# Kernel optimization log

Measured on AMD Instinct MI355X. Metric: run time of the kernel, lower is better.

Reference implementation:

```python
import jax, jax.numpy as jnp
import numpy as np

B, LQ, LK, D = 4, 2048, 2048, 512
EPS = 1e-8  # torch cosine_similarity eps


def setup_inputs() -> dict:
    key = jax.random.key(0)
    ks = jax.random.split(key, 8)
    s = 1.0 / np.sqrt(D)
    return {
        "query": jax.random.normal(ks[0], (B, LQ, D), jnp.float32),
        "key": jax.random.normal(ks[1], (B, LK, D), jnp.float32),
        "value": jax.random.normal(ks[2], (B, LK, D), jnp.float32),
        "Wq": jax.random.normal(ks[3], (D, D), jnp.float32) * s,
        "bq": jax.random.normal(ks[4], (D,), jnp.float32) * s,
        "Wk": jax.random.normal(ks[5], (D, D), jnp.float32) * s,
        "bk": jax.random.normal(ks[6], (D,), jnp.float32) * s,
        "scoring_weights": jnp.ones((3,), jnp.float32) / 3.0,
    }


def reference(query, key, value, Wq, bq, Wk, bk, scoring_weights):
    # fused tanh-QK transforms (torch Linear: x @ W.T + b)
    q = jnp.tanh(jnp.einsum('bqd,ed->bqe', query, Wq) + bq)  # [B,LQ,D]
    k = jnp.tanh(jnp.einsum('bkd,ed->bke', key, Wk) + bk)    # [B,LK,D]

    dot = jnp.einsum('bqd,bkd->bqk', q, k)                   # [B,LQ,LK]
    qn = jnp.linalg.norm(q, axis=-1)                         # [B,LQ]
    kn = jnp.linalg.norm(k, axis=-1)                         # [B,LK]
    # cosine_similarity: dot / max(|q|*|k|, eps)
    cos = dot / jnp.maximum(qn[:, :, None] * kn[:, None, :], EPS)
    # -cdist (p=2): sqrt(|q|^2 + |k|^2 - 2 q.k), clamped at 0
    sq = jnp.maximum(qn[:, :, None] ** 2 + kn[:, None, :] ** 2 - 2.0 * dot, 0.0)
    euc = -jnp.sqrt(sq)

    w = jax.nn.softmax(scoring_weights)
    scores = w[0] * dot + w[1] * cos + w[2] * euc
    attn = jax.nn.softmax(scores, axis=-1)                   # [B,LQ,LK]
    context = jnp.einsum('bqk,bkd->bqd', attn, value)        # [B,LQ,D]
    return context, attn
```

## Files before the change

### kernel.cpp

```cpp
#include <hip/hip_runtime.h>
#include <cstdint>
#include <cstddef>

namespace {

constexpr int BATCH = 4;
constexpr int LQ = 2048;
constexpr int LK = 2048;
constexpr int D = 512;
constexpr int MQ = BATCH * LQ;

using f16 = _Float16;
typedef _Float16 f16x8 __attribute__((ext_vector_type(8)));
typedef _Float16 f16x4 __attribute__((ext_vector_type(4)));
typedef float f32x4 __attribute__((ext_vector_type(4)));

__device__ __forceinline__ f16x8 cvt8(const float4 a, const float4 b) {
  f16x8 h;
  h[0] = (f16)a.x; h[1] = (f16)a.y; h[2] = (f16)a.z; h[3] = (f16)a.w;
  h[4] = (f16)b.x; h[5] = (f16)b.y; h[6] = (f16)b.z; h[7] = (f16)b.w;
  return h;
}

typedef __attribute__((address_space(1))) const void gas_void;
typedef __attribute__((address_space(3))) void las_void;
__device__ __forceinline__ void gload_lds16(const void* g, void* l) {
  __builtin_amdgcn_global_load_lds((gas_void*)g, (las_void*)l, 16, 0, 0);
}

__global__ __launch_bounds__(256) void prep_kernel(
    const float* __restrict__ query, const float* __restrict__ keyp,
    const float* __restrict__ value, const float* __restrict__ Wq,
    const float* __restrict__ Wk, const float* __restrict__ bq,
    const float* __restrict__ bk, f16* __restrict__ qh, f16* __restrict__ kh,
    float* __restrict__ qnsqp, float* __restrict__ knsqp,
    f16* __restrict__ vt) {
  __shared__ __align__(16) char smem[21504];
  const int bid0 = blockIdx.x;
  const int t = threadIdx.x;

  if (bid0 >= 512) {
    const int bid = bid0 - 512;
    const int kt = bid & 31;
    const int dt = (bid >> 5) & 7;
    const int b = bid >> 8;
    const int k0 = kt * 64, d0 = dt * 64;
    f16(*T)[72] = reinterpret_cast<f16(*)[72]>(smem);
#pragma unroll
    for (int i = 0; i < 4; ++i) {
      const int u = t + i * 256;
      const int k = u >> 4;
      const int d4 = (u & 15) << 2;
      float4 x = *reinterpret_cast<const float4*>(
          value + (size_t)(b * LK + k0 + k) * D + d0 + d4);
      T[d4 + 0][k] = (f16)x.x;
      T[d4 + 1][k] = (f16)x.y;
      T[d4 + 2][k] = (f16)x.z;
      T[d4 + 3][k] = (f16)x.w;
    }
    __syncthreads();
#pragma unroll
    for (int i = 0; i < 2; ++i) {
      const int u = t + i * 256;
      const int d = u >> 3;
      const int k8 = (u & 7) << 3;
      f16x8 h = *reinterpret_cast<const f16x8*>(&T[d][k8]);
      *reinterpret_cast<f16x8*>(vt + (size_t)(b * D + d0 + d) * LK + k0 + k8) =
          h;
    }
    return;
  }

  const int which = bid0 >> 8;
  const float* __restrict__ X = which ? keyp : query;
  const float* __restrict__ W = which ? Wk : Wq;
  const float* __restrict__ bias = which ? bk : bq;
  f16* __restrict__ out = which ? kh : qh;
  float* __restrict__ nsqp = which ? knsqp : qnsqp;

  const int bid = bid0 & 255;
  const int tm = bid & 63;
  const int tn = bid >> 6;
  const int brow = tm * 128, bcol = tn * 128;
  const int lane = t & 63;
  const int wid = t >> 6;
  const int wr = (wid >> 1) * 64, wc = (wid & 1) * 64;
  const int lr = lane & 15;
  const int lk = (lane >> 4) << 3;
  const int g4 = (lane >> 4) << 2;

  f16(*As)[40] = reinterpret_cast<f16(*)[40]>(smem);
  f16(*Bs)[40] = reinterpret_cast<f16(*)[40]>(smem + 10240);
  float(*s_ss)[2] = reinterpret_cast<float(*)[2]>(smem + 20480);

  f32x4 acc[4][4] = {};

  for (int k0 = 0; k0 < D; k0 += 32) {
#pragma unroll
    for (int i = 0; i < 2; ++i) {
      const int u = t + i * 256;
      const int r = u >> 2;
      const int c8 = (u & 3) << 3;
      const float4* pa =
          reinterpret_cast<const float4*>(X + (size_t)(brow + r) * D + k0 + c8);
      *reinterpret_cast<f16x8*>(&As[r][c8]) = cvt8(pa[0], pa[1]);
      const float4* pb =
          reinterpret_cast<const float4*>(W + (size_t)(bcol + r) * D + k0 + c8);
      *reinterpret_cast<f16x8*>(&Bs[r][c8]) = cvt8(pb[0], pb[1]);
    }
    __syncthreads();
    f16x8 af[4], bf[4];
#pragma unroll
    for (int m = 0; m < 4; ++m)
      af[m] = *reinterpret_cast<const f16x8*>(&As[wr + m * 16 + lr][lk]);
#pragma unroll
    for (int n = 0; n < 4; ++n)
      bf[n] = *reinterpret_cast<const f16x8*>(&Bs[wc + n * 16 + lr][lk]);
#pragma unroll
    for (int m = 0; m < 4; ++m)
#pragma unroll
      for (int n = 0; n < 4; ++n)
        acc[m][n] =
            __builtin_amdgcn_mfma_f32_16x16x32_f16(bf[n], af[m], acc[m][n], 0, 0, 0);
    __syncthreads();
  }

  float4 bv[4];
#pragma unroll
  for (int n = 0; n < 4; ++n)
    bv[n] = *reinterpret_cast<const float4*>(&bias[bcol + wc + n * 16 + g4]);

#pragma unroll
  for (int m = 0; m < 4; ++m) {
    const int row = brow + wr + m * 16 + lr;
    float ss = 0.f;
#pragma unroll
    for (int n = 0; n < 4; ++n) {
      float th[4];
#pragma unroll
      for (int r = 0; r < 4; ++r) {
        th[r] = tanhf(acc[m][n][r] + ((const float*)&bv[n])[r]);
        ss = fmaf(th[r], th[r], ss);
      }
      f16x4 h4;
      h4[0] = (f16)th[0]; h4[1] = (f16)th[1];
      h4[2] = (f16)th[2]; h4[3] = (f16)th[3];
      *reinterpret_cast<f16x4*>(out + (size_t)row * D + bcol + wc + n * 16 + g4) =
          h4;
    }
    ss += __shfl_xor(ss, 16);
    ss += __shfl_xor(ss, 32);
    if (lane < 16) s_ss[wr + m * 16 + lr][wid & 1] = ss;
  }
  __syncthreads();
  if (t < 128) nsqp[(size_t)(brow + t) * 4 + tn] = s_ss[t][0] + s_ss[t][1];
}

template <bool RAW16>
__global__ __launch_bounds__(256, 4) void scores_kernel(
    const f16* __restrict__ qh, const f16* __restrict__ kh,
    const float* __restrict__ qnsqp, const float* __restrict__ knsqp,
    const float* __restrict__ sw, float* __restrict__ attn,
    f16* __restrict__ sraw, float2* __restrict__ tstats) {
  const int bid0 = blockIdx.x;
  const int bid = (bid0 & 7) * 128 + (bid0 >> 3);
  const int tn = bid & 15;
  const int tm = (bid >> 4) & 15;
  const int b = bid >> 8;
  const int brow = tm * 128, bcol = tn * 128;
  const int t = threadIdx.x;
  const int lane = t & 63;
  const int wid = t >> 6;
  const int wr = (wid >> 1) * 64, wc = (wid & 1) * 64;
  const int lr = lane & 15;
  const int lk = (lane >> 4) << 3;
  const int g4 = (lane >> 4) << 2;

  __shared__ f16 As[128 * 64];
  __shared__ f16 Bs[128 * 64];
  __shared__ float s_m[128][2];
  __shared__ float s_l[128][2];

  f32x4 acc[4][4] = {};

  const int srow = lane >> 3;
  const int scol = ((lane & 7) ^ srow) << 4;
  const char* aBase = (const char*)(qh + (size_t)(b * LQ + brow) * D);
  const char* bBase = (const char*)(kh + (size_t)(b * LK + bcol) * D);
  const int swz = (lr & 7) << 4;

  for (int k0 = 0; k0 < D; k0 += 64) {
#pragma unroll
    for (int i = 0; i < 4; ++i) {
      const int chunk = wid * 4 + i;
      const int row = chunk * 8 + srow;
      gload_lds16(aBase + (size_t)row * (D * 2) + k0 * 2 + scol,
                  (char*)As + chunk * 1024);
      gload_lds16(bBase + (size_t)row * (D * 2) + k0 * 2 + scol,
                  (char*)Bs + chunk * 1024);
    }
    __syncthreads();
    f16x8 af[2][4], bf[2][4];
#pragma unroll
    for (int h = 0; h < 2; ++h) {
      const int cb = h * 64 + lk * 2;
#pragma unroll
      for (int m = 0; m < 4; ++m)
        af[h][m] = *(const f16x8*)((const char*)As + (wr + m * 16 + lr) * 128 +
                                   (cb ^ swz));
#pragma unroll
      for (int n = 0; n < 4; ++n)
        bf[h][n] = *(const f16x8*)((const char*)Bs + (wc + n * 16 + lr) * 128 +
                                   (cb ^ swz));
    }
#pragma unroll
    for (int h = 0; h < 2; ++h)
#pragma unroll
      for (int m = 0; m < 4; ++m)
#pragma unroll
        for (int n = 0; n < 4; ++n)
          acc[m][n] = __builtin_amdgcn_mfma_f32_16x16x32_f16(bf[h][n], af[h][m],
                                                             acc[m][n], 0, 0, 0);
    __syncthreads();
  }

  const float s0 = sw[0], s1 = sw[1], s2 = sw[2];
  const float smx = fmaxf(s0, fmaxf(s1, s2));
  float w0 = __expf(s0 - smx), w1 = __expf(s1 - smx), w2 = __expf(s2 - smx);
  const float winv = 1.f / (w0 + w1 + w2);
  w0 *= winv; w1 *= winv; w2 *= winv;

  float qn2_[4], w1rq[4];
#pragma unroll
  for (int m = 0; m < 4; ++m) {
    const float4 qp = *reinterpret_cast<const float4*>(
        &qnsqp[(size_t)(b * LQ + brow + wr + m * 16 + lr) * 4]);
    const float v = (qp.x + qp.y) + (qp.z + qp.w);
    qn2_[m] = v;
    w1rq[m] = w1 * rsqrtf(fmaxf(v, 1e-16f));
  }
  float kn2[4][4], rk[4][4];
#pragma unroll
  for (int n = 0; n < 4; ++n) {
#pragma unroll
    for (int r = 0; r < 4; ++r) {
      const int col = bcol + wc + n * 16 + g4 + r;
      const float4 kp = *reinterpret_cast<const float4*>(
          &knsqp[(size_t)(b * LK + col) * 4]);
      const float v = (kp.x + kp.y) + (kp.z + kp.w);
      kn2[n][r] = v;
      rk[n][r] = rsqrtf(fmaxf(v, 1e-16f));
    }
  }

#pragma unroll
  for (int m = 0; m < 4; ++m) {
    const int rl = wr + m * 16 + lr;
    const int row = brow + rl;
    float mx = -3.4e38f;
#pragma unroll
    for (int n = 0; n < 4; ++n) {
      float4 o;
#pragma unroll
      for (int r = 0; r < 4; ++r) {
        const float dot = acc[m][n][r];
        const float qk2 = qn2_[m] + kn2[n][r];
        const float st = sqrtf(fmaxf(qk2 - 2.f * dot, 0.f));
        const float c = fmaf(w1rq[m], rk[n][r], w0);
        const float s = fmaf(dot, c, -w2 * st);
        ((float*)&o)[r] = s;
        acc[m][n][r] = s;
        mx = fmaxf(mx, s);
      }
      if constexpr (!RAW16) {
        *reinterpret_cast<float4*>(attn + (size_t)(b * LQ + row) * LK + bcol +
                                   wc + n * 16 + g4) = o;
      }
    }
    mx = fmaxf(mx, __shfl_xor(mx, 16));
    mx = fmaxf(mx, __shfl_xor(mx, 32));
    if (lane < 16) s_m[rl][wid & 1] = mx;
  }
  __syncthreads();

#pragma unroll
  for (int m = 0; m < 4; ++m) {
    const int rl = wr + m * 16 + lr;
    const int row = brow + rl;
    const float Mt = fmaxf(s_m[rl][0], s_m[rl][1]);
    float es = 0.f;
#pragma unroll
    for (int n = 0; n < 4; ++n) {
      float e0 = __expf(acc[m][n][0] - Mt);
      float e1 = __expf(acc[m][n][1] - Mt);
      float e2 = __expf(acc[m][n][2] - Mt);
      float e3 = __expf(acc[m][n][3] - Mt);
      es += (e0 + e1) + (e2 + e3);
      if constexpr (RAW16) {
        f16x4 h4;
        h4[0] = (f16)e0; h4[1] = (f16)e1; h4[2] = (f16)e2; h4[3] = (f16)e3;
        *reinterpret_cast<f16x4*>(sraw + (size_t)(b * LQ + row) * LK + bcol +
                                  wc + n * 16 + g4) = h4;
      }
    }
    es += __shfl_xor(es, 16);
    es += __shfl_xor(es, 32);
    if (lane < 16) s_l[rl][wid & 1] = es;
  }
  __syncthreads();
  if (t < 128) {
    tstats[(size_t)(b * LQ + brow + t) * 16 + tn] =
        make_float2(fmaxf(s_m[t][0], s_m[t][1]), s_l[t][0] + s_l[t][1]);
  }
}

__global__ __launch_bounds__(256) void normalize_kernel(
    float* __restrict__ attn, const float2* __restrict__ tstats) {
  const int row = blockIdx.x;
  const int t = threadIdx.x;
  __shared__ float sM, sI;
  if (t < 16) {
    float2 st = tstats[(size_t)row * 16 + t];
    float M = st.x;
    M = fmaxf(M, __shfl_xor(M, 8));
    M = fmaxf(M, __shfl_xor(M, 4));
    M = fmaxf(M, __shfl_xor(M, 2));
    M = fmaxf(M, __shfl_xor(M, 1));
    float l = st.y * __expf(st.x - M);
    l += __shfl_xor(l, 8);
    l += __shfl_xor(l, 4);
    l += __shfl_xor(l, 2);
    l += __shfl_xor(l, 1);
    if (t == 0) { sM = M; sI = 1.f / l; }
  }
  __syncthreads();
  const float M = sM, invL = sI;
  float* rp = attn + (size_t)row * LK + t * 8;
  float4 v0 = *reinterpret_cast<const float4*>(rp);
  float4 v1 = *reinterpret_cast<const float4*>(rp + 4);
  v0.x = __expf(v0.x - M) * invL; v0.y = __expf(v0.y - M) * invL;
  v0.z = __expf(v0.z - M) * invL; v0.w = __expf(v0.w - M) * invL;
  v1.x = __expf(v1.x - M) * invL; v1.y = __expf(v1.y - M) * invL;
  v1.z = __expf(v1.z - M) * invL; v1.w = __expf(v1.w - M) * invL;
  *reinterpret_cast<float4*>(rp) = v0;
  *reinterpret_cast<float4*>(rp + 4) = v1;
}

template <bool NORM>
__global__ __launch_bounds__(512, 4) void pv_kernel(
    float* __restrict__ attnf, const f16* __restrict__ sraw,
    const f16* __restrict__ vt, const float2* __restrict__ tstats,
    float* __restrict__ ctx) {
  const int bid0 = blockIdx.x;
  const int bid = (bid0 & 7) * 64 + (bid0 >> 3);
  const int tn = bid & 3;
  const int tm = (bid >> 2) & 31;
  const int b = bid >> 7;
  const int brow = tm * 64, bcol = tn * 128;
  const int t = threadIdx.x;
  const int lane = t & 63;
  const int wid = t >> 6;
  const int wr = (wid >> 1) * 16, wc = (wid & 1) * 64;
  const int lr = lane & 15;
  const int lk = (lane >> 4) << 3;
  const int g4 = (lane >> 4) << 2;

  __shared__ f16 As[2][64 * 64];
  __shared__ f16 Bs[2][128 * 64];
  __shared__ f16 sScale[64][17];

  f32x4 acc[4] = {};

  const int srow = lane >> 3;
  const int scol = ((lane & 7) ^ srow) << 4;
  const size_t arow0 = (size_t)(b * LQ + brow);
  const char* bBase = (const char*)(vt + (size_t)(b * D + bcol) * LK);
  const int swz = (lr & 7) << 4;

  const int arow = t >> 3;
  const int c16 = (t & 7) << 4;
  const int csrc = c16 ^ ((arow & 7) << 4);
  const char* aRow =
      (const char*)sraw + (arow0 + arow) * (size_t)LK * 2 + csrc;

  if constexpr (NORM) {
    if (t < 256) {
      const int prow = t >> 2;
      const int j4 = (t & 3) * 4;
      const float4* tp =
          reinterpret_cast<const float4*>(&tstats[(arow0 + prow) * 16 + j4]);
      const float4 a = tp[0], c = tp[1];
      float m_ = fmaxf(fmaxf(a.x, a.z), fmaxf(c.x, c.z));
      m_ = fmaxf(m_, __shfl_xor(m_, 1));
      m_ = fmaxf(m_, __shfl_xor(m_, 2));
      float l_ = a.y * __expf(a.x - m_) + a.w * __expf(a.z - m_) +
                 c.y * __expf(c.x - m_) + c.w * __expf(c.z - m_);
      l_ += __shfl_xor(l_, 1);
      l_ += __shfl_xor(l_, 2);
      const float invL = 1.f / l_;
      sScale[prow][j4 + 0] = (f16)(__expf(a.x - m_) * invL);
      sScale[prow][j4 + 1] = (f16)(__expf(a.z - m_) * invL);
      sScale[prow][j4 + 2] = (f16)(__expf(c.x - m_) * invL);
      sScale[prow][j4 + 3] = (f16)(__expf(c.z - m_) * invL);
    }
    __syncthreads();
  }

#define PV_STAGE_B(bufi, kk)                                                 \
  _Pragma("unroll") for (int i_ = 0; i_ < 2; ++i_) {                         \
    const int chunk_ = wid * 2 + i_;                                         \
    const int row_ = chunk_ * 8 + srow;                                      \
    gload_lds16(bBase + (size_t)row_ * (LK * 2) + (kk)*2 + scol,             \
                (char*)Bs[bufi] + chunk_ * 1024);                            \
  }

#define PV_STAGE_A_NORM(bufi, kk, hreg)                                      \
  {                                                                          \
    const f16 sch_ = sScale[arow][(kk) >> 7];                                \
    const f16x8 scv_ = {sch_, sch_, sch_, sch_, sch_, sch_, sch_, sch_};     \
    const f16x8 hv_ = (hreg)*scv_;                                           \
    *(f16x8*)((char*)As[bufi] + arow * 128 + c16) = hv_;                     \
    if (((kk) >> 9) == tn) {                                                 \
      float4 e0_, e1_;                                                       \
      e0_.x = (float)hv_[0]; e0_.y = (float)hv_[1];                          \
      e0_.z = (float)hv_[2]; e0_.w = (float)hv_[3];                          \
      e1_.x = (float)hv_[4]; e1_.y = (float)hv_[5];                          \
      e1_.z = (float)hv_[6]; e1_.w = (float)hv_[7];                          \
      float* op_ = attnf + (arow0 + arow) * LK + (kk) + (csrc >> 1);         \
      *reinterpret_cast<float4*>(op_) = e0_;                                 \
      *reinterpret_cast<float4*>(op_ + 4) = e1_;                             \
    }                                                                        \
  }

#define PV_STAGE_A_F32(bufi, kk)                                             \
  {                                                                          \
    const float4* ps_ = (const float4*)((const char*)attnf +                 \
                                        ((arow0 + arow) * LK + (kk)) * 4 +   \
                                        csrc * 2);                           \
    *(f16x8*)((char*)As[bufi] + arow * 128 + c16) = cvt8(ps_[0], ps_[1]);    \
  }

  f16x8 hnext;
  if constexpr (NORM) {
    f16x8 h0 = *(const f16x8*)(aRow);
    PV_STAGE_B(0, 0);
    PV_STAGE_A_NORM(0, 0, h0);
    hnext = *(const f16x8*)(aRow + 64 * 2);
  } else {
    PV_STAGE_B(0, 0);
    PV_STAGE_A_F32(0, 0);
  }
  __syncthreads();

  int cur = 0;
  for (int k0 = 0; k0 < LK; k0 += 64) {
    const int kn = k0 + 64;
    if (kn < LK) {
      PV_STAGE_B(cur ^ 1, kn);
      if constexpr (NORM) {
        PV_STAGE_A_NORM(cur ^ 1, kn, hnext);
        if (kn + 64 < LK) hnext = *(const f16x8*)(aRow + (kn + 64) * 2);
      } else {
        PV_STAGE_A_F32(cur ^ 1, kn);
      }
    }
    f16x8 af[2], bf[2][4];
#pragma unroll
    for (int h = 0; h < 2; ++h) {
      const int cb = h * 64 + lk * 2;
      af[h] =
          *(const f16x8*)((const char*)As[cur] + (wr + lr) * 128 + (cb ^ swz));
#pragma unroll
      for (int n = 0; n < 4; ++n)
        bf[h][n] = *(const f16x8*)((const char*)Bs[cur] +
                                   (wc + n * 16 + lr) * 128 + (cb ^ swz));
    }
#pragma unroll
    for (int h = 0; h < 2; ++h)
#pragma unroll
      for (int n = 0; n < 4; ++n)
        acc[n] = __builtin_amdgcn_mfma_f32_16x16x32_f16(bf[h][n], af[h],
                                                        acc[n], 0, 0, 0);
    __syncthreads();
    cur ^= 1;
  }
#undef PV_STAGE_B
#undef PV_STAGE_A_NORM
#undef PV_STAGE_A_F32

  const int row = brow + wr + lr;
  float* rowp = ctx + (size_t)(b * LQ + row) * D + bcol + wc;
#pragma unroll
  for (int n = 0; n < 4; ++n) {
    float4 o;
    o.x = acc[n][0]; o.y = acc[n][1];
    o.z = acc[n][2]; o.w = acc[n][3];
    *reinterpret_cast<float4*>(rowp + n * 16 + g4) = o;
  }
}

}

extern "C" void kernel_launch(void* const* d_in, const int* in_sizes, int n_in,
                              void* d_out, int out_size, void* d_ws,
                              size_t ws_size, hipStream_t stream) {
  const float* query = (const float*)d_in[0];
  const float* key = (const float*)d_in[1];
  const float* value = (const float*)d_in[2];
  const float* Wq = (const float*)d_in[3];
  const float* bq = (const float*)d_in[4];
  const float* Wk = (const float*)d_in[5];
  const float* bk = (const float*)d_in[6];
  const float* sw = (const float*)d_in[7];

  float* ctx = (float*)d_out;
  float* attn = (float*)d_out + (size_t)BATCH * LQ * D;

  char* ws = (char*)d_ws;
  f16* vt = (f16*)ws;
  f16* qh = (f16*)(ws + (size_t)(8u << 20));
  f16* kh = (f16*)(ws + (size_t)(16u << 20));
  float* qnsqp = (float*)(ws + (size_t)(24u << 20));
  float* knsqp = qnsqp + (size_t)MQ * 4;
  float2* tstats = (float2*)(ws + (size_t)(25u << 20));
  f16* sraw = (f16*)(ws + (size_t)(26u << 20));
  const size_t ws_needed =
      ((size_t)(26u << 20)) + (size_t)BATCH * LQ * LK * sizeof(f16);
  const bool useA16 = ws_size >= ws_needed;

  prep_kernel<<<1536, 256, 0, stream>>>(query, key, value, Wq, Wk, bq, bk, qh,
                                        kh, qnsqp, knsqp, vt);
  if (useA16) {
    scores_kernel<true><<<1024, 256, 0, stream>>>(qh, kh, qnsqp, knsqp, sw,
                                                  attn, sraw, tstats);
    pv_kernel<true><<<512, 512, 0, stream>>>(attn, sraw, vt, tstats, ctx);
  } else {
    scores_kernel<false><<<1024, 256, 0, stream>>>(qh, kh, qnsqp, knsqp, sw,
                                                   attn, sraw, tstats);
    normalize_kernel<<<MQ, 256, 0, stream>>>(attn, tstats);
    pv_kernel<false><<<512, 512, 0, stream>>>(attn, sraw, vt, tstats, ctx);
  }
}
```

Before: 102.6 us.

## Shrink PV kernel to two waves with 64x64 register tiles per wave

The PV kernel goes from 8 waves (512 threads), each computing a 16x64 output tile, to 2 waves (128 threads), each computing a 64x64 tile with a 4x4 array of MFMA accumulators. Each thread now stages four A rows and eight B chunks per k-step, and the softmax scale prep is spread across all 128 threads. This gives more operand reuse per LDS fragment load and fewer barriers per unit of work. In exchange, each CU has fewer waves to hide latency, register pressure goes up, and the global-to-LDS staging is serialized across fewer threads.

```diff
diff --git a/kernel.cpp b/kernel.cpp
--- a/kernel.cpp
+++ b/kernel.cpp
@@ -347,7 +347,7 @@
 }
 
 template <bool NORM>
-__global__ __launch_bounds__(512, 4) void pv_kernel(
+__global__ __launch_bounds__(128) void pv_kernel(
     float* __restrict__ attnf, const f16* __restrict__ sraw,
     const f16* __restrict__ vt, const float2* __restrict__ tstats,
     float* __restrict__ ctx) {
@@ -360,7 +360,7 @@
   const int t = threadIdx.x;
   const int lane = t & 63;
   const int wid = t >> 6;
-  const int wr = (wid >> 1) * 16, wc = (wid & 1) * 64;
+  const int wc = wid * 64;
   const int lr = lane & 15;
   const int lk = (lane >> 4) << 3;
   const int g4 = (lane >> 4) << 2;
@@ -369,7 +369,7 @@
   __shared__ f16 Bs[2][128 * 64];
   __shared__ f16 sScale[64][17];
 
-  f32x4 acc[4] = {};
+  f32x4 acc[4][4] = {};
 
   const int srow = lane >> 3;
   const int scol = ((lane & 7) ^ srow) << 4;
@@ -377,75 +377,87 @@
   const char* bBase = (const char*)(vt + (size_t)(b * D + bcol) * LK);
   const int swz = (lr & 7) << 4;
 
-  const int arow = t >> 3;
+  const int urow0 = t >> 3;
   const int c16 = (t & 7) << 4;
-  const int csrc = c16 ^ ((arow & 7) << 4);
-  const char* aRow =
-      (const char*)sraw + (arow0 + arow) * (size_t)LK * 2 + csrc;
+  const int csrc = c16 ^ ((urow0 & 7) << 4);
+  const char* aBase = (const char*)sraw + arow0 * (size_t)LK * 2 + csrc;
 
   if constexpr (NORM) {
-    if (t < 256) {
-      const int prow = t >> 2;
-      const int j4 = (t & 3) * 4;
-      const float4* tp =
-          reinterpret_cast<const float4*>(&tstats[(arow0 + prow) * 16 + j4]);
-      const float4 a = tp[0], c = tp[1];
-      float m_ = fmaxf(fmaxf(a.x, a.z), fmaxf(c.x, c.z));
-      m_ = fmaxf(m_, __shfl_xor(m_, 1));
-      m_ = fmaxf(m_, __shfl_xor(m_, 2));
-      float l_ = a.y * __expf(a.x - m_) + a.w * __expf(a.z - m_) +
-                 c.y * __expf(c.x - m_) + c.w * __expf(c.z - m_);
-      l_ += __shfl_xor(l_, 1);
-      l_ += __shfl_xor(l_, 2);
-      const float invL = 1.f / l_;
-      sScale[prow][j4 + 0] = (f16)(__expf(a.x - m_) * invL);
-      sScale[prow][j4 + 1] = (f16)(__expf(a.z - m_) * invL);
-      sScale[prow][j4 + 2] = (f16)(__expf(c.x - m_) * invL);
-      sScale[prow][j4 + 3] = (f16)(__expf(c.z - m_) * invL);
-    }
+    const int prow = t >> 1;
+    const int j8 = (t & 1) * 8;
+    const float4* tp =
+        reinterpret_cast<const float4*>(&tstats[(arow0 + prow) * 16 + j8]);
+    float4 tv[4];
+    float m_ = -3.4e38f;
+#pragma unroll
+    for (int j = 0; j < 4; ++j) {
+      tv[j] = tp[j];
+      m_ = fmaxf(m_, fmaxf(tv[j].x, tv[j].z));
+    }
+    m_ = fmaxf(m_, __shfl_xor(m_, 1));
+    float e[8];
+    float l_ = 0.f;
+#pragma unroll
+    for (int j = 0; j < 4; ++j) {
+      e[2 * j] = __expf(tv[j].x - m_);
+      e[2 * j + 1] = __expf(tv[j].z - m_);
+      l_ += tv[j].y * e[2 * j] + tv[j].w * e[2 * j + 1];
+    }
+    l_ += __shfl_xor(l_, 1);
+    const float invL = 1.f / l_;
+#pragma unroll
+    for (int j = 0; j < 8; ++j) sScale[prow][j8 + j] = (f16)(e[j] * invL);
     __syncthreads();
   }
 
 #define PV_STAGE_B(bufi, kk)                                                 \
-  _Pragma("unroll") for (int i_ = 0; i_ < 2; ++i_) {                         \
-    const int chunk_ = wid * 2 + i_;                                         \
+  _Pragma("unroll") for (int i_ = 0; i_ < 8; ++i_) {                         \
+    const int chunk_ = wid * 8 + i_;                                         \
     const int row_ = chunk_ * 8 + srow;                                      \
     gload_lds16(bBase + (size_t)row_ * (LK * 2) + (kk)*2 + scol,             \
                 (char*)Bs[bufi] + chunk_ * 1024);                            \
   }
 
 #define PV_STAGE_A_NORM(bufi, kk, hreg)                                      \
-  {                                                                          \
-    const f16 sch_ = sScale[arow][(kk) >> 7];                                \
+  _Pragma("unroll") for (int i_ = 0; i_ < 4; ++i_) {                         \
+    const int row_ = urow0 + i_ * 16;                                        \
+    const f16 sch_ = sScale[row_][(kk) >> 7];                                \
     const f16x8 scv_ = {sch_, sch_, sch_, sch_, sch_, sch_, sch_, sch_};     \
-    const f16x8 hv_ = (hreg)*scv_;                                           \
-    *(f16x8*)((char*)As[bufi] + arow * 128 + c16) = hv_;                     \
+    const f16x8 hv_ = (hreg)[i_] * scv_;                                     \
+    *(f16x8*)((char*)As[bufi] + row_ * 128 + c16) = hv_;                     \
     if (((kk) >> 9) == tn) {                                                 \
       float4 e0_, e1_;                                                       \
       e0_.x = (float)hv_[0]; e0_.y = (float)hv_[1];                          \
       e0_.z = (float)hv_[2]; e0_.w = (float)hv_[3];                          \
       e1_.x = (float)hv_[4]; e1_.y = (float)hv_[5];                          \
       e1_.z = (float)hv_[6]; e1_.w = (float)hv_[7];                          \
-      float* op_ = attnf + (arow0 + arow) * LK + (kk) + (csrc >> 1);         \
+      float* op_ = attnf + (arow0 + row_) * LK + (kk) + (csrc >> 1);         \
       *reinterpret_cast<float4*>(op_) = e0_;                                 \
       *reinterpret_cast<float4*>(op_ + 4) = e1_;                             \
     }                                                                        \
   }
 
+#define PV_LOAD_A(hreg, kk)                                                  \
+  _Pragma("unroll") for (int i_ = 0; i_ < 4; ++i_) {                         \
+    (hreg)[i_] = *(const f16x8*)(aBase + (size_t)(urow0 + i_ * 16) *         \
+                                             (LK * 2) + (kk)*2);             \
+  }
+
 #define PV_STAGE_A_F32(bufi, kk)                                             \
-  {                                                                          \
+  _Pragma("unroll") for (int i_ = 0; i_ < 4; ++i_) {                         \
+    const int row_ = urow0 + i_ * 16;                                        \
     const float4* ps_ = (const float4*)((const char*)attnf +                 \
-                                        ((arow0 + arow) * LK + (kk)) * 4 +   \
+                                        ((arow0 + row_) * LK + (kk)) * 4 +   \
                                         csrc * 2);                           \
-    *(f16x8*)((char*)As[bufi] + arow * 128 + c16) = cvt8(ps_[0], ps_[1]);    \
-  }
-
-  f16x8 hnext;
+    *(f16x8*)((char*)As[bufi] + row_ * 128 + c16) = cvt8(ps_[0], ps_[1]);    \
+  }
+
+  f16x8 hq[4];
   if constexpr (NORM) {
-    f16x8 h0 = *(const f16x8*)(aRow);
+    PV_LOAD_A(hq, 0);
     PV_STAGE_B(0, 0);
-    PV_STAGE_A_NORM(0, 0, h0);
-    hnext = *(const f16x8*)(aRow + 64 * 2);
+    PV_STAGE_A_NORM(0, 0, hq);
+    PV_LOAD_A(hq, 64);
   } else {
     PV_STAGE_B(0, 0);
     PV_STAGE_A_F32(0, 0);
@@ -458,18 +470,20 @@
     if (kn < LK) {
       PV_STAGE_B(cur ^ 1, kn);
       if constexpr (NORM) {
-        PV_STAGE_A_NORM(cur ^ 1, kn, hnext);
-        if (kn + 64 < LK) hnext = *(const f16x8*)(aRow + (kn + 64) * 2);
+        PV_STAGE_A_NORM(cur ^ 1, kn, hq);
+        if (kn + 64 < LK) PV_LOAD_A(hq, kn + 64);
       } else {
         PV_STAGE_A_F32(cur ^ 1, kn);
       }
     }
-    f16x8 af[2], bf[2][4];
+    f16x8 af[2][4], bf[2][4];
 #pragma unroll
     for (int h = 0; h < 2; ++h) {
       const int cb = h * 64 + lk * 2;
-      af[h] =
-          *(const f16x8*)((const char*)As[cur] + (wr + lr) * 128 + (cb ^ swz));
+#pragma unroll
+      for (int m = 0; m < 4; ++m)
+        af[h][m] = *(const f16x8*)((const char*)As[cur] +
+                                   (m * 16 + lr) * 128 + (cb ^ swz));
 #pragma unroll
       for (int n = 0; n < 4; ++n)
         bf[h][n] = *(const f16x8*)((const char*)Bs[cur] +
@@ -478,24 +492,30 @@
 #pragma unroll
     for (int h = 0; h < 2; ++h)
 #pragma unroll
-      for (int n = 0; n < 4; ++n)
-        acc[n] = __builtin_amdgcn_mfma_f32_16x16x32_f16(bf[h][n], af[h],
-                                                        acc[n], 0, 0, 0);
+      for (int m = 0; m < 4; ++m)
+#pragma unroll
+        for (int n = 0; n < 4; ++n)
+          acc[m][n] = __builtin_amdgcn_mfma_f32_16x16x32_f16(
+              bf[h][n], af[h][m], acc[m][n], 0, 0, 0);
     __syncthreads();
     cur ^= 1;
   }
 #undef PV_STAGE_B
 #undef PV_STAGE_A_NORM
+#undef PV_LOAD_A
 #undef PV_STAGE_A_F32
 
-  const int row = brow + wr + lr;
-  float* rowp = ctx + (size_t)(b * LQ + row) * D + bcol + wc;
-#pragma unroll
-  for (int n = 0; n < 4; ++n) {
-    float4 o;
-    o.x = acc[n][0]; o.y = acc[n][1];
-    o.z = acc[n][2]; o.w = acc[n][3];
-    *reinterpret_cast<float4*>(rowp + n * 16 + g4) = o;
+#pragma unroll
+  for (int m = 0; m < 4; ++m) {
+    const int row = brow + m * 16 + lr;
+    float* rowp = ctx + (size_t)(b * LQ + row) * D + bcol + wc;
+#pragma unroll
+    for (int n = 0; n < 4; ++n) {
+      float4 o;
+      o.x = acc[m][n][0]; o.y = acc[m][n][1];
+      o.z = acc[m][n][2]; o.w = acc[m][n][3];
+      *reinterpret_cast<float4*>(rowp + n * 16 + g4) = o;
+    }
   }
 }
 
@@ -533,11 +553,11 @@
   if (useA16) {
     scores_kernel<true><<<1024, 256, 0, stream>>>(qh, kh, qnsqp, knsqp, sw,
                                                   attn, sraw, tstats);
-    pv_kernel<true><<<512, 512, 0, stream>>>(attn, sraw, vt, tstats, ctx);
+    pv_kernel<true><<<512, 128, 0, stream>>>(attn, sraw, vt, tstats, ctx);
   } else {
     scores_kernel<false><<<1024, 256, 0, stream>>>(qh, kh, qnsqp, knsqp, sw,
                                                    attn, sraw, tstats);
     normalize_kernel<<<MQ, 256, 0, stream>>>(attn, tstats);
-    pv_kernel<false><<<512, 512, 0, stream>>>(attn, sraw, vt, tstats, ctx);
-  }
-}
+    pv_kernel<false><<<512, 128, 0, stream>>>(attn, sraw, vt, tstats, ctx);
+  }
+}
```

Result: slower. 113.0 us (+10.1%).

## Halve PV block to 4 warps with 32x64 warp tiles, single LDS buffer

Applied to the files above, without the earlier changes.

The PV kernel now runs 256 threads per block instead of 512. Each warp computes a 32x64 output tile with two A fragments, so every loaded B fragment feeds twice as many MFMAs. The LDS double buffering is removed: each iteration stages into a single buffer, syncs, computes and syncs again, while the next A chunk is prefetched into registers. This raises register-level reuse and halves LDS use, at the cost of less overlap between loads and compute and fewer waves per block.

```diff
diff --git a/kernel.cpp b/kernel.cpp
--- a/kernel.cpp
+++ b/kernel.cpp
@@ -347,7 +347,7 @@
 }
 
 template <bool NORM>
-__global__ __launch_bounds__(512, 4) void pv_kernel(
+__global__ __launch_bounds__(256, 2) void pv_kernel(
     float* __restrict__ attnf, const f16* __restrict__ sraw,
     const f16* __restrict__ vt, const float2* __restrict__ tstats,
     float* __restrict__ ctx) {
@@ -360,16 +360,17 @@
   const int t = threadIdx.x;
   const int lane = t & 63;
   const int wid = t >> 6;
-  const int wr = (wid >> 1) * 16, wc = (wid & 1) * 64;
+  const int wrw = (wid >> 1) * 32;
+  const int wcw = (wid & 1) * 64;
   const int lr = lane & 15;
   const int lk = (lane >> 4) << 3;
   const int g4 = (lane >> 4) << 2;
 
-  __shared__ f16 As[2][64 * 64];
-  __shared__ f16 Bs[2][128 * 64];
+  __shared__ f16 As[64 * 64];
+  __shared__ f16 Bs[128 * 64];
   __shared__ f16 sScale[64][17];
 
-  f32x4 acc[4] = {};
+  f32x4 acc[2][4] = {};
 
   const int srow = lane >> 3;
   const int scol = ((lane & 7) ^ srow) << 4;
@@ -377,125 +378,128 @@
   const char* bBase = (const char*)(vt + (size_t)(b * D + bcol) * LK);
   const int swz = (lr & 7) << 4;
 
-  const int arow = t >> 3;
+  const int urow0 = t >> 3;
   const int c16 = (t & 7) << 4;
-  const int csrc = c16 ^ ((arow & 7) << 4);
-  const char* aRow =
-      (const char*)sraw + (arow0 + arow) * (size_t)LK * 2 + csrc;
+  const int csrc = c16 ^ ((urow0 & 7) << 4);
+  const char* aBase = (const char*)sraw + arow0 * (size_t)LK * 2 + csrc;
 
   if constexpr (NORM) {
-    if (t < 256) {
-      const int prow = t >> 2;
-      const int j4 = (t & 3) * 4;
-      const float4* tp =
-          reinterpret_cast<const float4*>(&tstats[(arow0 + prow) * 16 + j4]);
-      const float4 a = tp[0], c = tp[1];
-      float m_ = fmaxf(fmaxf(a.x, a.z), fmaxf(c.x, c.z));
-      m_ = fmaxf(m_, __shfl_xor(m_, 1));
-      m_ = fmaxf(m_, __shfl_xor(m_, 2));
-      float l_ = a.y * __expf(a.x - m_) + a.w * __expf(a.z - m_) +
-                 c.y * __expf(c.x - m_) + c.w * __expf(c.z - m_);
-      l_ += __shfl_xor(l_, 1);
-      l_ += __shfl_xor(l_, 2);
-      const float invL = 1.f / l_;
-      sScale[prow][j4 + 0] = (f16)(__expf(a.x - m_) * invL);
-      sScale[prow][j4 + 1] = (f16)(__expf(a.z - m_) * invL);
-      sScale[prow][j4 + 2] = (f16)(__expf(c.x - m_) * invL);
-      sScale[prow][j4 + 3] = (f16)(__expf(c.z - m_) * invL);
-    }
-    __syncthreads();
-  }
-
-#define PV_STAGE_B(bufi, kk)                                                 \
-  _Pragma("unroll") for (int i_ = 0; i_ < 2; ++i_) {                         \
-    const int chunk_ = wid * 2 + i_;                                         \
+    const int prow = t >> 2;
+    const int j4 = (t & 3) * 4;
+    const float4* tp =
+        reinterpret_cast<const float4*>(&tstats[(arow0 + prow) * 16 + j4]);
+    const float4 a = tp[0], c = tp[1];
+    float m_ = fmaxf(fmaxf(a.x, a.z), fmaxf(c.x, c.z));
+    m_ = fmaxf(m_, __shfl_xor(m_, 1));
+    m_ = fmaxf(m_, __shfl_xor(m_, 2));
+    float l_ = a.y * __expf(a.x - m_) + a.w * __expf(a.z - m_) +
+               c.y * __expf(c.x - m_) + c.w * __expf(c.z - m_);
+    l_ += __shfl_xor(l_, 1);
+    l_ += __shfl_xor(l_, 2);
+    const float invL = 1.f / l_;
+    sScale[prow][j4 + 0] = (f16)(__expf(a.x - m_) * invL);
+    sScale[prow][j4 + 1] = (f16)(__expf(a.z - m_) * invL);
+    sScale[prow][j4 + 2] = (f16)(__expf(c.x - m_) * invL);
+    sScale[prow][j4 + 3] = (f16)(__expf(c.z - m_) * invL);
+    __syncthreads();
+  }
+
+#define PV_STAGE_B(kk)                                                       \
+  _Pragma("unroll") for (int i_ = 0; i_ < 4; ++i_) {                         \
+    const int chunk_ = wid * 4 + i_;                                         \
     const int row_ = chunk_ * 8 + srow;                                      \
     gload_lds16(bBase + (size_t)row_ * (LK * 2) + (kk)*2 + scol,             \
-                (char*)Bs[bufi] + chunk_ * 1024);                            \
-  }
-
-#define PV_STAGE_A_NORM(bufi, kk, hreg)                                      \
-  {                                                                          \
-    const f16 sch_ = sScale[arow][(kk) >> 7];                                \
+                (char*)Bs + chunk_ * 1024);                                  \
+  }
+
+#define PV_LOAD_A(hreg, kk)                                                  \
+  _Pragma("unroll") for (int i_ = 0; i_ < 2; ++i_) {                         \
+    (hreg)[i_] = *(const f16x8*)(aBase + (size_t)(urow0 + i_ * 32) *         \
+                                             (LK * 2) + (kk)*2);             \
+  }
+
+#define PV_STAGE_A_NORM(kk, hreg)                                            \
+  _Pragma("unroll") for (int i_ = 0; i_ < 2; ++i_) {                         \
+    const int row_ = urow0 + i_ * 32;                                        \
+    const f16 sch_ = sScale[row_][(kk) >> 7];                                \
     const f16x8 scv_ = {sch_, sch_, sch_, sch_, sch_, sch_, sch_, sch_};     \
-    const f16x8 hv_ = (hreg)*scv_;                                           \
-    *(f16x8*)((char*)As[bufi] + arow * 128 + c16) = hv_;                     \
+    const f16x8 hv_ = (hreg)[i_] * scv_;                                     \
+    *(f16x8*)((char*)As + row_ * 128 + c16) = hv_;                           \
     if (((kk) >> 9) == tn) {                                                 \
       float4 e0_, e1_;                                                       \
       e0_.x = (float)hv_[0]; e0_.y = (float)hv_[1];                          \
       e0_.z = (float)hv_[2]; e0_.w = (float)hv_[3];                          \
       e1_.x = (float)hv_[4]; e1_.y = (float)hv_[5];                          \
       e1_.z = (float)hv_[6]; e1_.w = (float)hv_[7];                          \
-      float* op_ = attnf + (arow0 + arow) * LK + (kk) + (csrc >> 1);         \
+      float* op_ = attnf + (arow0 + row_) * LK + (kk) + (csrc >> 1);         \
       *reinterpret_cast<float4*>(op_) = e0_;                                 \
       *reinterpret_cast<float4*>(op_ + 4) = e1_;                             \
     }                                                                        \
   }
 
-#define PV_STAGE_A_F32(bufi, kk)                                             \
-  {                                                                          \
+#define PV_STAGE_A_F32(kk)                                                   \
+  _Pragma("unroll") for (int i_ = 0; i_ < 2; ++i_) {                         \
+    const int row_ = urow0 + i_ * 32;                                        \
     const float4* ps_ = (const float4*)((const char*)attnf +                 \
-                                        ((arow0 + arow) * LK + (kk)) * 4 +   \
+                                        ((arow0 + row_) * LK + (kk)) * 4 +   \
                                         csrc * 2);                           \
-    *(f16x8*)((char*)As[bufi] + arow * 128 + c16) = cvt8(ps_[0], ps_[1]);    \
-  }
-
-  f16x8 hnext;
-  if constexpr (NORM) {
-    f16x8 h0 = *(const f16x8*)(aRow);
-    PV_STAGE_B(0, 0);
-    PV_STAGE_A_NORM(0, 0, h0);
-    hnext = *(const f16x8*)(aRow + 64 * 2);
-  } else {
-    PV_STAGE_B(0, 0);
-    PV_STAGE_A_F32(0, 0);
-  }
-  __syncthreads();
-
-  int cur = 0;
+    *(f16x8*)((char*)As + row_ * 128 + c16) = cvt8(ps_[0], ps_[1]);          \
+  }
+
+  f16x8 hq[2];
+  if constexpr (NORM) PV_LOAD_A(hq, 0);
+
   for (int k0 = 0; k0 < LK; k0 += 64) {
-    const int kn = k0 + 64;
-    if (kn < LK) {
-      PV_STAGE_B(cur ^ 1, kn);
-      if constexpr (NORM) {
-        PV_STAGE_A_NORM(cur ^ 1, kn, hnext);
-        if (kn + 64 < LK) hnext = *(const f16x8*)(aRow + (kn + 64) * 2);
-      } else {
-        PV_STAGE_A_F32(cur ^ 1, kn);
-      }
-    }
-    f16x8 af[2], bf[2][4];
+    PV_STAGE_B(k0);
+    if constexpr (NORM) {
+      f16x8 hn[2];
+      if (k0 + 64 < LK) PV_LOAD_A(hn, k0 + 64);
+      PV_STAGE_A_NORM(k0, hq);
+      hq[0] = hn[0];
+      hq[1] = hn[1];
+    } else {
+      PV_STAGE_A_F32(k0);
+    }
+    __syncthreads();
+    f16x8 af[2][2], bf[2][4];
 #pragma unroll
     for (int h = 0; h < 2; ++h) {
       const int cb = h * 64 + lk * 2;
-      af[h] =
-          *(const f16x8*)((const char*)As[cur] + (wr + lr) * 128 + (cb ^ swz));
+#pragma unroll
+      for (int m = 0; m < 2; ++m)
+        af[h][m] = *(const f16x8*)((const char*)As + (wrw + m * 16 + lr) * 128 +
+                                   (cb ^ swz));
 #pragma unroll
       for (int n = 0; n < 4; ++n)
-        bf[h][n] = *(const f16x8*)((const char*)Bs[cur] +
-                                   (wc + n * 16 + lr) * 128 + (cb ^ swz));
+        bf[h][n] = *(const f16x8*)((const char*)Bs + (wcw + n * 16 + lr) * 128 +
+                                   (cb ^ swz));
     }
 #pragma unroll
     for (int h = 0; h < 2; ++h)
 #pragma unroll
-      for (int n = 0; n < 4; ++n)
-        acc[n] = __builtin_amdgcn_mfma_f32_16x16x32_f16(bf[h][n], af[h],
-                                                        acc[n], 0, 0, 0);
-    __syncthreads();
-    cur ^= 1;
+      for (int m = 0; m < 2; ++m)
+#pragma unroll
+        for (int n = 0; n < 4; ++n)
+          acc[m][n] = __builtin_amdgcn_mfma_f32_16x16x32_f16(
+              bf[h][n], af[h][m], acc[m][n], 0, 0, 0);
+    __syncthreads();
   }
 #undef PV_STAGE_B
+#undef PV_LOAD_A
 #undef PV_STAGE_A_NORM
 #undef PV_STAGE_A_F32
 
-  const int row = brow + wr + lr;
-  float* rowp = ctx + (size_t)(b * LQ + row) * D + bcol + wc;
-#pragma unroll
-  for (int n = 0; n < 4; ++n) {
-    float4 o;
-    o.x = acc[n][0]; o.y = acc[n][1];
-    o.z = acc[n][2]; o.w = acc[n][3];
-    *reinterpret_cast<float4*>(rowp + n * 16 + g4) = o;
+#pragma unroll
+  for (int m = 0; m < 2; ++m) {
+    const int row = brow + wrw + m * 16 + lr;
+    float* rowp = ctx + (size_t)(b * LQ + row) * D + bcol + wcw;
+#pragma unroll
+    for (int n = 0; n < 4; ++n) {
+      float4 o;
+      o.x = acc[m][n][0]; o.y = acc[m][n][1];
+      o.z = acc[m][n][2]; o.w = acc[m][n][3];
+      *reinterpret_cast<float4*>(rowp + n * 16 + g4) = o;
+    }
   }
 }
 
@@ -533,11 +537,11 @@
   if (useA16) {
     scores_kernel<true><<<1024, 256, 0, stream>>>(qh, kh, qnsqp, knsqp, sw,
                                                   attn, sraw, tstats);
-    pv_kernel<true><<<512, 512, 0, stream>>>(attn, sraw, vt, tstats, ctx);
+    pv_kernel<true><<<512, 256, 0, stream>>>(attn, sraw, vt, tstats, ctx);
   } else {
     scores_kernel<false><<<1024, 256, 0, stream>>>(qh, kh, qnsqp, knsqp, sw,
                                                    attn, sraw, tstats);
     normalize_kernel<<<MQ, 256, 0, stream>>>(attn, tstats);
-    pv_kernel<false><<<512, 512, 0, stream>>>(attn, sraw, vt, tstats, ctx);
-  }
-}
+    pv_kernel<false><<<512, 256, 0, stream>>>(attn, sraw, vt, tstats, ctx);
+  }
+}
```

Result: slower. 106.7 us (+3.9%).
